# Optimization experiments

Hardware: AMD Instinct MI355X
Metric: run time of the kernel (lower is better)

Reference implementation:

```python
import jax, jax.numpy as jnp
import numpy as np

B, L, D, H = 2, 2048, 1024, 16
NEG = -1.0e9


def setup_inputs() -> dict:
    key = jax.random.key(0)
    k1, k2, k3, k4 = jax.random.split(key, 4)
    query = jax.random.normal(k1, (B, L, D), dtype=jnp.float32)
    key_t = jax.random.normal(k2, (B, L, D), dtype=jnp.float32)
    value = jax.random.normal(k3, (B, L, D), dtype=jnp.float32)
    # Conv1D c_proj params: w ~ N(0, 0.02), b = 0   (nx=D -> nf=D)
    w_proj = 0.02 * jax.random.normal(k4, (D, D), dtype=jnp.float32)
    b_proj = jnp.zeros((D,), dtype=jnp.float32)
    return {"query": query, "key": key_t, "value": value,
            "w_proj": w_proj, "b_proj": b_proj, "n_head": H}


def reference(query, key, value, w_proj, b_proj, n_head):
    b, l, d = query.shape
    dh = d // n_head
    # split_heads -> [B, H, L, dh]
    q = query.reshape(b, l, n_head, dh).transpose(0, 2, 1, 3)
    k = key.reshape(b, l, n_head, dh).transpose(0, 2, 1, 3)
    v = value.reshape(b, l, n_head, dh).transpose(0, 2, 1, 3)
    # scores: [B, H, L, L], scaled by sqrt(head_dim) (v.size(-1) after split)
    w = jnp.einsum("bhqd,bhkd->bhqk", q, k) / jnp.sqrt(jnp.float32(dh))
    # one_dir_visible=True: multiplicative causal mask, w*m + (-1e9)*(1-m)
    m = jnp.tril(jnp.ones((l, l), dtype=w.dtype))[None, None]
    w = w * m + NEG * (1.0 - m)
    p = jax.nn.softmax(w, axis=-1)  # attn_dropout p=0 -> identity
    a = jnp.einsum("bhqk,bhkd->bhqd", p, v)  # [B, H, L, dh]
    # merge_heads -> [B, L, D]
    a = a.transpose(0, 2, 1, 3).reshape(b, l, d)
    # c_proj (Conv1D == dense): resid_dropout p=0 -> identity
    return a @ w_proj + b_proj
```

## Files before the change

kernel.cpp:

```cpp
#include <hip/hip_runtime.h>
#include <hip/hip_bf16.h>

constexpr int kB  = 2;
constexpr int kL  = 2048;
constexpr int kD  = 1024;
constexpr int kH  = 16;
constexpr int kDH = 64;
constexpr int kM  = kB * kL;

typedef _Float16 half8 __attribute__((ext_vector_type(8)));
typedef float    f32x4 __attribute__((ext_vector_type(4)));

constexpr size_t kKhOff = 0;
constexpr size_t kVtOff = 8388608;
constexpr size_t kAhOff = 16777216;
constexpr size_t kWtOff = 25165824;
constexpr size_t kWsNeed = 27262976;

__device__ __forceinline__ void load16_lds(const void* g, void* l) {
    __builtin_amdgcn_global_load_lds((__attribute__((address_space(1))) void*)(g),
                                     (__attribute__((address_space(3))) void*)(l),
                                     16, 0, 0);
}

__global__ __launch_bounds__(256) void conv_fused(const float* __restrict__ K,
                                                  const float* __restrict__ V,
                                                  const float* __restrict__ W,
                                                  _Float16* __restrict__ Kh,
                                                  _Float16* __restrict__ Vt,
                                                  _Float16* __restrict__ Wt) {
    __shared__ _Float16 Ts[64][65];
    const int t = threadIdx.x;
    const int bid = blockIdx.x;

    if (bid < 2048) {
        size_t i = ((size_t)bid * 256 + t) * 8;
        float4 f0 = *(const float4*)(K + i);
        float4 f1 = *(const float4*)(K + i + 4);
        half8 h;
        h[0] = (_Float16)f0.x; h[1] = (_Float16)f0.y; h[2] = (_Float16)f0.z; h[3] = (_Float16)f0.w;
        h[4] = (_Float16)f1.x; h[5] = (_Float16)f1.y; h[6] = (_Float16)f1.z; h[7] = (_Float16)f1.w;
        *(half8*)(Kh + i) = h;
    } else if (bid < 3072) {
        const int b2 = bid - 2048;
        const int lt = b2 & 31, h = (b2 >> 5) & 15, b = b2 >> 9;
        for (int p = 0; p < 16; ++p) {
            int i = p * 256 + t;
            int r = i >> 6, c = i & 63;
            Ts[r][c] = (_Float16)V[((size_t)(b * kL + lt * 64 + r)) * kD + h * kDH + c];
        }
        __syncthreads();
        for (int p = 0; p < 16; ++p) {
            int i = p * 256 + t;
            int r = i >> 6, c = i & 63;
            Vt[((size_t)(b * kH + h) * kDH + r) * kL + lt * 64 + c] = Ts[c][r];
        }
    } else {
        const int b3 = bid - 3072;
        const int nt = b3 & 15, kt = b3 >> 4;
        const int k0 = kt * 64, n0 = nt * 64;
        for (int p = 0; p < 16; ++p) {
            int i = p * 256 + t;
            int r = i >> 6, c = i & 63;
            Ts[r][c] = (_Float16)W[(size_t)(k0 + r) * kD + n0 + c];
        }
        __syncthreads();
        for (int p = 0; p < 16; ++p) {
            int i = p * 256 + t;
            int r = i >> 6, c = i & 63;
            Wt[(size_t)(n0 + r) * kD + k0 + c] = Ts[c][r];
        }
    }
}

__global__ __launch_bounds__(256, 4) void flash_kernel(const float* __restrict__ Q,
                                                       const _Float16* __restrict__ Kh,
                                                       const _Float16* __restrict__ Vt,
                                                       _Float16* __restrict__ Ah) {
    __shared__ __align__(16) _Float16 Ks[2][64 * 64];
    __shared__ __align__(16) _Float16 Vs[2][64 * 64];
    __shared__ __align__(16) _Float16 Ps[4][16 * 64];

    const int t = threadIdx.x;
    const int lane = t & 63, w = t >> 6;
    const int l15 = lane & 15, quad = lane >> 4;
    const int lhi = l15 >> 3, llo = l15 & 7;
    const int bid = blockIdx.x;
    const int bh = bid & 31;
    const int qt = 31 - (bid >> 5);
    const int b = bh >> 4, h = bh & 15;
    const int Tq = qt + 1;
    const int qrow0 = qt * 64 + w * 16;
    const size_t hoff = (size_t)h * kDH;

    const int srow = w * 16 + (lane >> 3);
    const int sj   = ((lane & 7) - (lane >> 3)) & 7;
    const _Float16* kgp = Kh + (size_t)(b * kL) * kD + hoff + sj * 8;
    const _Float16* vgp = Vt + (size_t)(bh * kDH) * kL + sj * 8;

    half8 aq[2];
    #pragma unroll
    for (int kc = 0; kc < 2; ++kc) {
        const float* qp = Q + (size_t)(b * kL + qrow0 + l15) * kD + hoff + kc * 32 + quad * 8;
        float4 f0 = *(const float4*)qp;
        float4 f1 = *(const float4*)(qp + 4);
        half8 hq;
        hq[0] = (_Float16)(f0.x * 0.125f); hq[1] = (_Float16)(f0.y * 0.125f);
        hq[2] = (_Float16)(f0.z * 0.125f); hq[3] = (_Float16)(f0.w * 0.125f);
        hq[4] = (_Float16)(f1.x * 0.125f); hq[5] = (_Float16)(f1.y * 0.125f);
        hq[6] = (_Float16)(f1.z * 0.125f); hq[7] = (_Float16)(f1.w * 0.125f);
        aq[kc] = hq;
    }

    half8 ones;
    #pragma unroll
    for (int i = 0; i < 8; ++i) ones[i] = (_Float16)1.0f;

    f32x4 o[4];
    f32x4 lsum = (f32x4){0.f, 0.f, 0.f, 0.f};
    #pragma unroll
    for (int nt = 0; nt < 4; ++nt) o[nt] = (f32x4){0.f, 0.f, 0.f, 0.f};

    _Float16* pp = Ps[w];

    constexpr float kLog2e = 1.4426950408889634f;
    constexpr float kBias  = -11.541560327111707f;

    load16_lds(kgp + (size_t)srow * kD,       &Ks[0][(w * 16) * 64]);
    load16_lds(kgp + (size_t)(srow + 8) * kD, &Ks[0][(w * 16 + 8) * 64]);
    load16_lds(vgp + (size_t)srow * kL,       &Vs[0][(w * 16) * 64]);
    load16_lds(vgp + (size_t)(srow + 8) * kL, &Vs[0][(w * 16 + 8) * 64]);

    for (int kt = 0; kt < Tq; ++kt) {
        const int cur = kt & 1;
        __syncthreads();

        if (kt + 1 < Tq) {
            const int kb1 = (kt + 1) * 64;
            load16_lds(kgp + (size_t)(kb1 + srow) * kD,     &Ks[cur ^ 1][(w * 16) * 64]);
            load16_lds(kgp + (size_t)(kb1 + srow + 8) * kD, &Ks[cur ^ 1][(w * 16 + 8) * 64]);
            load16_lds(vgp + (size_t)srow * kL + kb1,       &Vs[cur ^ 1][(w * 16) * 64]);
            load16_lds(vgp + (size_t)(srow + 8) * kL + kb1, &Vs[cur ^ 1][(w * 16 + 8) * 64]);
        }

        f32x4 s[4];
        #pragma unroll
        for (int nt = 0; nt < 4; ++nt) {
            s[nt] = (f32x4){0.f, 0.f, 0.f, 0.f};
            #pragma unroll
            for (int kc = 0; kc < 2; ++kc) {
                const int r = nt * 16 + l15;
                const int slot = (quad + 4 * kc + l15) & 7;
                half8 bk = *(half8*)&Ks[cur][r * 64 + slot * 8];
                s[nt] = __builtin_amdgcn_mfma_f32_16x16x32_f16(aq[kc], bk, s[nt], 0, 0, 0);
            }
        }

        if (kt == Tq - 1) {
            const int kb = kt * 64;
            const int row = qrow0 + quad * 4;
            #pragma unroll
            for (int nt = 0; nt < 4; ++nt)
                #pragma unroll
                for (int r = 0; r < 4; ++r)
                    if (kb + nt * 16 + l15 > row + r) s[nt][r] = -1.0e30f;
        }

        #pragma unroll
        for (int nt = 0; nt < 4; ++nt)
            #pragma unroll
            for (int r = 0; r < 4; ++r) {
                float p = exp2f(fmaf(s[nt][r], kLog2e, kBias));
                const int prow = quad * 4 + r;
                const int slot = (nt * 2 + lhi + prow) & 7;
                pp[prow * 64 + slot * 8 + llo] = (_Float16)p;
            }

        half8 ap[2];
        #pragma unroll
        for (int kc = 0; kc < 2; ++kc) {
            const int slot = (kc * 4 + quad + l15) & 7;
            ap[kc] = *(half8*)&pp[l15 * 64 + slot * 8];
        }

        #pragma unroll
        for (int nt = 0; nt < 4; ++nt)
            #pragma unroll
            for (int kc = 0; kc < 2; ++kc) {
                const int r = nt * 16 + l15;
                const int slot = (quad + 4 * kc + l15) & 7;
                half8 bv = *(half8*)&Vs[cur][r * 64 + slot * 8];
                o[nt] = __builtin_amdgcn_mfma_f32_16x16x32_f16(ap[kc], bv, o[nt], 0, 0, 0);
            }
        lsum = __builtin_amdgcn_mfma_f32_16x16x32_f16(ap[0], ones, lsum, 0, 0, 0);
        lsum = __builtin_amdgcn_mfma_f32_16x16x32_f16(ap[1], ones, lsum, 0, 0, 0);
    }

    const size_t orow = (size_t)(b * kL + qrow0 + quad * 4);
    #pragma unroll
    for (int r = 0; r < 4; ++r) {
        float inv = 1.0f / lsum[r];
        #pragma unroll
        for (int nt = 0; nt < 4; ++nt)
            Ah[(orow + r) * kD + hoff + nt * 16 + l15] = (_Float16)(o[nt][r] * inv);
    }
}

__global__ __launch_bounds__(256, 2) void proj_half(const _Float16* __restrict__ Ah,
                                                    const _Float16* __restrict__ Wt,
                                                    const float* __restrict__ bias,
                                                    float* __restrict__ out) {
    constexpr int PAD = 72;
    __shared__ __align__(16) _Float16 As[128 * PAD];
    __shared__ __align__(16) _Float16 Bs[64 * PAD];

    const int t = threadIdx.x;
    const int lane = t & 63, w = t >> 6;
    const int l15 = lane & 15, quad = lane >> 4;
    const int m0 = blockIdx.x * 128, n0 = blockIdx.y * 64;
    const int wm = (w >> 1) * 64, wn = (w & 1) * 32;

    f32x4 c[4][2];
    #pragma unroll
    for (int i = 0; i < 4; ++i)
        #pragma unroll
        for (int j = 0; j < 2; ++j) c[i][j] = (f32x4){0.f, 0.f, 0.f, 0.f};

    for (int k0 = 0; k0 < kD; k0 += 64) {
        __syncthreads();
        #pragma unroll
        for (int p = 0; p < 4; ++p) {
            int idx = p * 256 + t;
            int row = idx >> 3, seg = idx & 7;
            *(half8*)&As[row * PAD + seg * 8] =
                *(const half8*)(Ah + (size_t)(m0 + row) * kD + k0 + seg * 8);
        }
        #pragma unroll
        for (int p = 0; p < 2; ++p) {
            int idx = p * 256 + t;
            int row = idx >> 3, seg = idx & 7;
            *(half8*)&Bs[row * PAD + seg * 8] =
                *(const half8*)(Wt + (size_t)(n0 + row) * kD + k0 + seg * 8);
        }
        __syncthreads();

        #pragma unroll
        for (int kc = 0; kc < 2; ++kc) {
            half8 a[4], bf[2];
            #pragma unroll
            for (int mt = 0; mt < 4; ++mt)
                a[mt] = *(half8*)&As[(wm + mt * 16 + l15) * PAD + kc * 32 + quad * 8];
            #pragma unroll
            for (int nt = 0; nt < 2; ++nt)
                bf[nt] = *(half8*)&Bs[(wn + nt * 16 + l15) * PAD + kc * 32 + quad * 8];
            #pragma unroll
            for (int mt = 0; mt < 4; ++mt)
                #pragma unroll
                for (int nt = 0; nt < 2; ++nt)
                    c[mt][nt] = __builtin_amdgcn_mfma_f32_16x16x32_f16(a[mt], bf[nt], c[mt][nt], 0, 0, 0);
        }
    }

    #pragma unroll
    for (int nt = 0; nt < 2; ++nt) {
        int n = n0 + wn + nt * 16 + l15;
        float bv = bias[n];
        #pragma unroll
        for (int mt = 0; mt < 4; ++mt) {
            int mrow = m0 + wm + mt * 16 + quad * 4;
            #pragma unroll
            for (int r = 0; r < 4; ++r)
                out[(size_t)(mrow + r) * kD + n] = c[mt][nt][r] + bv;
        }
    }
}

__global__ __launch_bounds__(256) void attn_kernel_f32(const float* __restrict__ Q,
                                                       const float* __restrict__ K,
                                                       const float* __restrict__ V,
                                                       float* __restrict__ A) {
    const int lane = threadIdx.x & 63;
    const int wave = threadIdx.x >> 6;
    const int tilesPerBH = kL / 4;
    const int bh = blockIdx.x / tilesPerBH;
    const int tile = blockIdx.x % tilesPerBH;
    const int b = bh / kH, h = bh % kH;
    const int qi = tile * 4 + wave;
    const size_t base = (size_t)b * kL * kD + (size_t)h * kDH;
    const float* kptr = K + base;
    const float* vptr = V + base;
    const float qd = Q[base + (size_t)qi * kD + lane] * 0.125f;
    float m = -3.0e38f, l = 0.0f, acc = 0.0f;
    for (int j = 0; j <= qi; ++j) {
        const float kd = kptr[(size_t)j * kD + lane];
        float s = qd * kd;
        #pragma unroll
        for (int off = 32; off; off >>= 1) s += __shfl_xor(s, off);
        const float mnew = fmaxf(m, s);
        const float corr = __expf(m - mnew);
        const float p = __expf(s - mnew);
        const float vd = vptr[(size_t)j * kD + lane];
        l = l * corr + p;
        acc = acc * corr + p * vd;
        m = mnew;
    }
    A[base + (size_t)qi * kD + lane] = acc / l;
}

__global__ __launch_bounds__(256) void proj_kernel_f32(const float* __restrict__ A,
                                                       const float* __restrict__ W,
                                                       const float* __restrict__ bias,
                                                       float* __restrict__ out) {
    __shared__ __align__(16) float As[16][64];
    __shared__ __align__(16) float Ws[16][64];
    const int t = threadIdx.x;
    const int m0 = blockIdx.x * 64, n0 = blockIdx.y * 64;
    const int tx = t & 15, ty = t >> 4;
    const int arow = t >> 2, acol4 = (t & 3) * 4;
    const int wrow = t >> 4, wcol4 = (t & 15) * 4;
    float c[4][4] = {};
    for (int k0 = 0; k0 < kD; k0 += 16) {
        const float4 av = *(const float4*)(A + (size_t)(m0 + arow) * kD + k0 + acol4);
        const float4 wv = *(const float4*)(W + (size_t)(k0 + wrow) * kD + n0 + wcol4);
        __syncthreads();
        As[acol4 + 0][arow] = av.x;
        As[acol4 + 1][arow] = av.y;
        As[acol4 + 2][arow] = av.z;
        As[acol4 + 3][arow] = av.w;
        *(float4*)&Ws[wrow][wcol4] = wv;
        __syncthreads();
        #pragma unroll
        for (int kk = 0; kk < 16; ++kk) {
            const float4 a = *(const float4*)&As[kk][ty * 4];
            const float4 wv2 = *(const float4*)&Ws[kk][tx * 4];
            c[0][0] += a.x * wv2.x; c[0][1] += a.x * wv2.y; c[0][2] += a.x * wv2.z; c[0][3] += a.x * wv2.w;
            c[1][0] += a.y * wv2.x; c[1][1] += a.y * wv2.y; c[1][2] += a.y * wv2.z; c[1][3] += a.y * wv2.w;
            c[2][0] += a.z * wv2.x; c[2][1] += a.z * wv2.y; c[2][2] += a.z * wv2.z; c[2][3] += a.z * wv2.w;
            c[3][0] += a.w * wv2.x; c[3][1] += a.w * wv2.y; c[3][2] += a.w * wv2.z; c[3][3] += a.w * wv2.w;
        }
    }
    const float4 bv = *(const float4*)(bias + n0 + tx * 4);
    #pragma unroll
    for (int i = 0; i < 4; ++i) {
        float4 o;
        o.x = c[i][0] + bv.x; o.y = c[i][1] + bv.y; o.z = c[i][2] + bv.z; o.w = c[i][3] + bv.w;
        *(float4*)(out + (size_t)(m0 + ty * 4 + i) * kD + n0 + tx * 4) = o;
    }
}

extern "C" void kernel_launch(void* const* d_in, const int* in_sizes, int n_in,
                              void* d_out, int out_size, void* d_ws, size_t ws_size,
                              hipStream_t stream) {
    const float* Q    = (const float*)d_in[0];
    const float* K    = (const float*)d_in[1];
    const float* V    = (const float*)d_in[2];
    const float* W    = (const float*)d_in[3];
    const float* bias = (const float*)d_in[4];
    float* out = (float*)d_out;

    if (ws_size >= kWsNeed) {
        char* ws = (char*)d_ws;
        _Float16* Kh = (_Float16*)(ws + kKhOff);
        _Float16* Vt = (_Float16*)(ws + kVtOff);
        _Float16* Ah = (_Float16*)(ws + kAhOff);
        _Float16* Wt = (_Float16*)(ws + kWtOff);

        conv_fused<<<dim3(3328), 256, 0, stream>>>(K, V, W, Kh, Vt, Wt);
        flash_kernel<<<dim3(1024), 256, 0, stream>>>(Q, Kh, Vt, Ah);
        proj_half<<<dim3(kM / 128, kD / 64), 256, 0, stream>>>(Ah, Wt, bias, out);
    } else {
        float* A = (float*)d_ws;
        attn_kernel_f32<<<dim3(kB * kH * (kL / 4)), 256, 0, stream>>>(Q, K, V, A);
        proj_kernel_f32<<<dim3(kM / 64, kD / 64), 256, 0, stream>>>(A, W, bias, out);
    }
}
```

Before: 160.0 us.

## Double-buffer projection GEMM with direct global-to-LDS loads and swizzled 64x64 tiles

Rewrites the output projection GEMM to use 64x64 block tiles instead of 128x64. Tiles are loaded with global_load_lds straight into double-buffered, XOR-swizzled shared memory, so the next K-tile loads while the current one is multiplied. Smaller tiles and the launch bound of 4 blocks per CU double the grid and raise occupancy. The trade is less register-level reuse per wave (one A fragment across four B fragments) and more total global traffic for the operand tiles.

Result: no change. 158.3 us (-1.1%).

```diff
diff --git a/kernel.cpp b/kernel.cpp
--- a/kernel.cpp
+++ b/kernel.cpp
@@ -206,72 +206,67 @@
     }
 }
 
-__global__ __launch_bounds__(256, 2) void proj_half(const _Float16* __restrict__ Ah,
+__global__ __launch_bounds__(256, 4) void proj_half(const _Float16* __restrict__ Ah,
                                                     const _Float16* __restrict__ Wt,
                                                     const float* __restrict__ bias,
                                                     float* __restrict__ out) {
-    constexpr int PAD = 72;
-    __shared__ __align__(16) _Float16 As[128 * PAD];
-    __shared__ __align__(16) _Float16 Bs[64 * PAD];
+    __shared__ __align__(16) _Float16 As[2][64 * 64];
+    __shared__ __align__(16) _Float16 Bs[2][64 * 64];
 
     const int t = threadIdx.x;
     const int lane = t & 63, w = t >> 6;
     const int l15 = lane & 15, quad = lane >> 4;
-    const int m0 = blockIdx.x * 128, n0 = blockIdx.y * 64;
-    const int wm = (w >> 1) * 64, wn = (w & 1) * 32;
-
-    f32x4 c[4][2];
-    #pragma unroll
-    for (int i = 0; i < 4; ++i)
-        #pragma unroll
-        for (int j = 0; j < 2; ++j) c[i][j] = (f32x4){0.f, 0.f, 0.f, 0.f};
-
-    for (int k0 = 0; k0 < kD; k0 += 64) {
-        __syncthreads();
-        #pragma unroll
-        for (int p = 0; p < 4; ++p) {
-            int idx = p * 256 + t;
-            int row = idx >> 3, seg = idx & 7;
-            *(half8*)&As[row * PAD + seg * 8] =
-                *(const half8*)(Ah + (size_t)(m0 + row) * kD + k0 + seg * 8);
-        }
-        #pragma unroll
-        for (int p = 0; p < 2; ++p) {
-            int idx = p * 256 + t;
-            int row = idx >> 3, seg = idx & 7;
-            *(half8*)&Bs[row * PAD + seg * 8] =
-                *(const half8*)(Wt + (size_t)(n0 + row) * kD + k0 + seg * 8);
-        }
-        __syncthreads();
+    const int m0 = blockIdx.x * 64, n0 = blockIdx.y * 64;
+
+    const int srow = w * 16 + (lane >> 3);
+    const int sj   = ((lane & 7) - (lane >> 3)) & 7;
+    const _Float16* agp = Ah + (size_t)(m0 + srow) * kD + sj * 8;
+    const _Float16* bgp = Wt + (size_t)(n0 + srow) * kD + sj * 8;
+
+    f32x4 c[4];
+    #pragma unroll
+    for (int nt = 0; nt < 4; ++nt) c[nt] = (f32x4){0.f, 0.f, 0.f, 0.f};
+
+    load16_lds(agp,                    &As[0][(w * 16) * 64]);
+    load16_lds(agp + (size_t)8 * kD,   &As[0][(w * 16 + 8) * 64]);
+    load16_lds(bgp,                    &Bs[0][(w * 16) * 64]);
+    load16_lds(bgp + (size_t)8 * kD,   &Bs[0][(w * 16 + 8) * 64]);
+
+    for (int kt = 0; kt < 16; ++kt) {
+        const int cur = kt & 1;
+        __syncthreads();
+
+        if (kt + 1 < 16) {
+            const int k1 = (kt + 1) * 64;
+            load16_lds(agp + k1,                  &As[cur ^ 1][(w * 16) * 64]);
+            load16_lds(agp + (size_t)8 * kD + k1, &As[cur ^ 1][(w * 16 + 8) * 64]);
+            load16_lds(bgp + k1,                  &Bs[cur ^ 1][(w * 16) * 64]);
+            load16_lds(bgp + (size_t)8 * kD + k1, &Bs[cur ^ 1][(w * 16 + 8) * 64]);
+        }
 
         #pragma unroll
         for (int kc = 0; kc < 2; ++kc) {
-            half8 a[4], bf[2];
-            #pragma unroll
-            for (int mt = 0; mt < 4; ++mt)
-                a[mt] = *(half8*)&As[(wm + mt * 16 + l15) * PAD + kc * 32 + quad * 8];
-            #pragma unroll
-            for (int nt = 0; nt < 2; ++nt)
-                bf[nt] = *(half8*)&Bs[(wn + nt * 16 + l15) * PAD + kc * 32 + quad * 8];
-            #pragma unroll
-            for (int mt = 0; mt < 4; ++mt)
-                #pragma unroll
-                for (int nt = 0; nt < 2; ++nt)
-                    c[mt][nt] = __builtin_amdgcn_mfma_f32_16x16x32_f16(a[mt], bf[nt], c[mt][nt], 0, 0, 0);
-        }
-    }
-
-    #pragma unroll
-    for (int nt = 0; nt < 2; ++nt) {
-        int n = n0 + wn + nt * 16 + l15;
-        float bv = bias[n];
-        #pragma unroll
-        for (int mt = 0; mt < 4; ++mt) {
-            int mrow = m0 + wm + mt * 16 + quad * 4;
-            #pragma unroll
-            for (int r = 0; r < 4; ++r)
-                out[(size_t)(mrow + r) * kD + n] = c[mt][nt][r] + bv;
-        }
+            const int arow = w * 16 + l15;
+            const int aslot = (kc * 4 + quad + l15) & 7;
+            half8 a = *(half8*)&As[cur][arow * 64 + aslot * 8];
+            #pragma unroll
+            for (int nt = 0; nt < 4; ++nt) {
+                const int brow = nt * 16 + l15;
+                const int bslot = (kc * 4 + quad + l15) & 7;
+                half8 bf = *(half8*)&Bs[cur][brow * 64 + bslot * 8];
+                c[nt] = __builtin_amdgcn_mfma_f32_16x16x32_f16(a, bf, c[nt], 0, 0, 0);
+            }
+        }
+    }
+
+    #pragma unroll
+    for (int nt = 0; nt < 4; ++nt) {
+        const int n = n0 + nt * 16 + l15;
+        const float bv = bias[n];
+        const int mrow = m0 + w * 16 + quad * 4;
+        #pragma unroll
+        for (int r = 0; r < 4; ++r)
+            out[(size_t)(mrow + r) * kD + n] = c[nt][r] + bv;
     }
 }
 
@@ -367,7 +362,7 @@
 
         conv_fused<<<dim3(3328), 256, 0, stream>>>(K, V, W, Kh, Vt, Wt);
         flash_kernel<<<dim3(1024), 256, 0, stream>>>(Q, Kh, Vt, Ah);
-        proj_half<<<dim3(kM / 128, kD / 64), 256, 0, stream>>>(Ah, Wt, bias, out);
+        proj_half<<<dim3(kM / 64, kD / 64), 256, 0, stream>>>(Ah, Wt, bias, out);
     } else {
         float* A = (float*)d_ws;
         attn_kernel_f32<<<dim3(kB * kH * (kL / 4)), 256, 0, stream>>>(Q, K, V, A);
```
